# Optimization experiments

Measured on AMD Instinct MI355X. Metric: run time of the kernel, lower is better.

Reference implementation:

```python
import jax, jax.numpy as jnp
import numpy as np

T, B, E, F = 2048, 8, 512, 2
N = E * F  # state dim = emb_dim * exp_factor


def setup_inputs() -> dict:
    key = jax.random.key(0)
    ks = jax.random.split(key, 14)
    x = jax.random.normal(ks[0], (T, B, E), dtype=jnp.float32)
    # in/out projections (torch Linear: y = x @ W.T + b; we store W already transposed)
    W_in = jax.random.normal(ks[1], (E, N), dtype=jnp.float32) / np.sqrt(E)
    b_in = jnp.zeros((N,), dtype=jnp.float32)
    W_out = jax.random.normal(ks[2], (N, E), dtype=jnp.float32) / np.sqrt(N)
    b_out = jnp.zeros((E,), dtype=jnp.float32)
    # LRU eigenvalue parameterization (r_min=0, r_max=1)
    u1 = jax.random.uniform(ks[3], (N,), dtype=jnp.float32, minval=1e-4, maxval=1.0)
    u2 = jax.random.uniform(ks[4], (N,), dtype=jnp.float32)
    nu_log = jnp.log(-0.5 * jnp.log(u1))
    theta_log = jnp.log(u2 * 2.0 * np.pi)
    gamma_log = jnp.log(jnp.sqrt(1.0 - jnp.exp(-jnp.exp(nu_log)) ** 2))
    B_real = jax.random.normal(ks[5], (N, N), dtype=jnp.float32) / np.sqrt(2 * E)
    B_imag = jax.random.normal(ks[6], (N, N), dtype=jnp.float32) / np.sqrt(2 * N)
    C_real = jax.random.normal(ks[7], (N, N), dtype=jnp.float32) / np.sqrt(N)
    C_imag = jax.random.normal(ks[8], (N, N), dtype=jnp.float32) / np.sqrt(N)
    D = jax.random.normal(ks[9], (N,), dtype=jnp.float32)
    return {"x": x, "W_in": W_in, "b_in": b_in, "W_out": W_out, "b_out": b_out,
            "nu_log": nu_log, "theta_log": theta_log, "gamma_log": gamma_log,
            "B_real": B_real, "B_imag": B_imag, "C_real": C_real, "C_imag": C_imag,
            "D": D}


def _bin_op(el1, el2):
    a_i, bu_i = el1
    a_j, bu_j = el2
    return (a_j * a_i, a_j * bu_i + bu_j)


def reference(x, W_in, b_in, W_out, b_out, nu_log, theta_log, gamma_log,
              B_real, B_imag, C_real, C_imag, D):
    u = x @ W_in + b_in                                   # [T,B,N] real
    Lam = jnp.exp(-jnp.exp(nu_log) + 1j * jnp.exp(theta_log))        # [N] complex
    B_norm = (B_real + 1j * B_imag) * jnp.exp(gamma_log)[:, None]    # [N,N]
    C = C_real + 1j * C_imag                                          # [N,N]
    # Bu[t,b,j] = sum_i B_norm[i,j] * u[t,b,i]  (matches einsum 'ij,kmi->kmj')
    Bu = jnp.einsum('ij,tbi->tbj', B_norm, u.astype(B_norm.dtype))   # [T,B,N]
    Lam_elems = jnp.broadcast_to(Lam, Bu.shape)                       # [T,B,N]
    # linear recurrence h_t = Lam * h_{t-1} + Bu_t via associative scan over time (axis 0)
    _, h = jax.lax.associative_scan(_bin_op, (Lam_elems, Bu), axis=0)
    y = (jnp.einsum('ij,tbi->tbj', C, h) + D * u).real                # [T,B,N]
    return y @ W_out + b_out                                          # [T,B,E]
```

## Files before the change

### kernel.cpp

```cpp
#include <hip/hip_runtime.h>
#include <hip/hip_bf16.h>

typedef __hip_bfloat16 bf16;
typedef __attribute__((ext_vector_type(8))) short bf16x8;
typedef __attribute__((ext_vector_type(4))) float f32x4;

#define T_DIM 2048
#define B_DIM 8
#define E_DIM 512
#define N_DIM 1024
#define M_ROWS (T_DIM * B_DIM)
#define NCHUNK 64
#define CLEN (T_DIM / NCHUNK)

__device__ __forceinline__ void gload16(const void* g, void* l) {
    __builtin_amdgcn_global_load_lds((const void __attribute__((address_space(1)))*)g,
                                     (void __attribute__((address_space(3)))*)l, 16, 0, 0);
}

__global__ void k_prep(const float* __restrict__ nu_log, const float* __restrict__ theta_log,
                       const float* __restrict__ gamma_log,
                       float* __restrict__ LamR, float* __restrict__ LamI, float* __restrict__ g) {
    int i = blockIdx.x * 256 + threadIdx.x;
    if (i < N_DIM) {
        float nu  = expf(nu_log[i]);
        float th  = expf(theta_log[i]);
        float mag = expf(-nu);
        LamR[i] = mag * cosf(th);
        LamI[i] = mag * sinf(th);
        g[i] = expf(gamma_log[i]);
    }
}

struct __align__(8) bf4 { bf16 v[4]; };
__global__ void k_conv_all(const float* __restrict__ x, const float* __restrict__ W_in,
                           const float* __restrict__ C_r, const float* __restrict__ C_i,
                           bf16* __restrict__ xb, bf16* __restrict__ Win_b,
                           bf16* __restrict__ Cr_b, bf16* __restrict__ Ci_b) {
    int id = blockIdx.x;
    const float* src; bf16* dst; float mul = 1.f; int base;
    if (id < 8192)      { src = x;    dst = xb;    base = id; }
    else if (id < 8704) { src = W_in; dst = Win_b; base = id - 8192; }
    else if (id < 9728) { src = C_r;  dst = Cr_b;  base = id - 8704; }
    else                { src = C_i;  dst = Ci_b;  base = id - 9728; mul = -1.f; }
    int i = base * 256 + threadIdx.x;
    float4 v = ((const float4*)src)[i];
    bf4 o;
    o.v[0] = __float2bfloat16(v.x * mul);
    o.v[1] = __float2bfloat16(v.y * mul);
    o.v[2] = __float2bfloat16(v.z * mul);
    o.v[3] = __float2bfloat16(v.w * mul);
    ((bf4*)dst)[i] = o;
}

__global__ void k_transpose_all(const float* __restrict__ B_r, const float* __restrict__ B_i,
                                const float* __restrict__ W_out, const float* __restrict__ gvec,
                                const float* __restrict__ Dvec,
                                bf16* __restrict__ BscT, bf16* __restrict__ WoT,
                                bf16* __restrict__ WoTD) {
    __shared__ float tile[32][33];
    int id = blockIdx.x;
    const float* in; bf16* out; const float* scale; int R, C, bx, by;
    if (id < 1024)      { in = B_r;   out = BscT;                      scale = gvec; R = 1024; C = 1024; bx = id & 31;          by = id >> 5; }
    else if (id < 2048) { int l = id - 1024; in = B_i; out = BscT + (size_t)1024 * 1024; scale = gvec; R = 1024; C = 1024; bx = l & 31; by = l >> 5; }
    else if (id < 2560) { int l = id - 2048; in = W_out; out = WoT;    scale = nullptr; R = 1024; C = 512; bx = l & 15; by = l >> 4; }
    else                { int l = id - 2560; in = W_out; out = WoTD;   scale = Dvec;   R = 1024; C = 512; bx = l & 15; by = l >> 4; }
    int tx = threadIdx.x & 31, ty = threadIdx.x >> 5;
    int r0 = by * 32, c0 = bx * 32;
#pragma unroll
    for (int i = 0; i < 32; i += 8) {
        int r = r0 + ty + i;
        float v = in[(size_t)r * C + c0 + tx];
        if (scale) v *= scale[r];
        tile[ty + i][tx] = v;
    }
    __syncthreads();
#pragma unroll
    for (int i = 0; i < 32; i += 8) {
        out[(size_t)(c0 + ty + i) * R + r0 + tx] = __float2bfloat16(tile[tx][ty + i]);
    }
}

__global__ void k_bias_bu(const float* __restrict__ b_in, const float* __restrict__ g,
                          const float* __restrict__ B_real, const float* __restrict__ B_imag,
                          float* __restrict__ c_bu) {
    int id = blockIdx.x;
    int jblk = id & 7, ic = id >> 3;
    int j = jblk * 256 + threadIdx.x;
    const float* B = (j < N_DIM) ? B_real : B_imag;
    int jj = j & (N_DIM - 1);
    float s = 0.f;
    for (int i = ic * 128; i < ic * 128 + 128; ++i)
        s = fmaf(b_in[i] * g[i], B[(size_t)i * N_DIM + jj], s);
    atomicAdd(&c_bu[j], s);
}

__global__ void k_bias_out(const float* __restrict__ b_out, const float* __restrict__ b_in,
                           const float* __restrict__ D, const float* __restrict__ W_out,
                           float* __restrict__ bo) {
    int id = blockIdx.x;
    int eblk = id & 1, ic = id >> 1;
    int e = eblk * 256 + threadIdx.x;
    float s = (ic == 0) ? b_out[e] : 0.f;
    for (int j = ic * 128; j < ic * 128 + 128; ++j)
        s = fmaf(b_in[j] * D[j], W_out[(size_t)j * E_DIM + e], s);
    atomicAdd(&bo[e], s);
}

template <bool ASPLIT, bool OUTF32, bool BIAS>
__device__ __forceinline__ void gemm_db_core(bf16* lds,
        const bf16* __restrict__ A0, const bf16* __restrict__ A1, int ksplit,
        int lda0, int lda1, const bf16* __restrict__ Bt, int ldb,
        void* __restrict__ outp, int ldo, const float* __restrict__ bias, int K,
        int bn, int bm) {
    const int tid = threadIdx.x;
    const int lane = tid & 63, w = tid >> 6;
    const int wr = w >> 1, wc = w & 1;
    const int fr = lane & 15, fq = lane >> 4;
    f32x4 acc[4][4] = {};
    const int nt = K / 32;

    auto stage = [&](int buf, int t) {
        int k0 = t * 32;
        const bf16* Ap = A0; int lda = lda0, ac = k0;
        if (ASPLIT && k0 >= ksplit) { Ap = A1; lda = lda1; ac = k0 - ksplit; }
        bf16* dst = lds + buf * 8192;
#pragma unroll
        for (int L = 0; L < 2; ++L) {
            int idx = L * 256 + tid;
            int rr = idx >> 2, s = idx & 3;
            int kk = (s ^ (rr & 3)) * 8;
            gload16(Ap + (size_t)(bm * 128 + rr) * lda + ac + kk, dst + idx * 8);
            gload16(Bt + (size_t)(bn * 128 + rr) * ldb + k0 + kk, dst + 4096 + idx * 8);
        }
    };

    stage(0, 0);
    __syncthreads();
    int cur = 0;
    for (int t = 0; t < nt; ++t) {
        if (t + 1 < nt) stage(cur ^ 1, t + 1);
        const bf16* bufA = lds + cur * 8192;
        const bf16* bufB = bufA + 4096;
        bf16x8 af[4], bfr[4];
#pragma unroll
        for (int i = 0; i < 4; ++i) {
            int rr = wr * 64 + i * 16 + fr;
            af[i] = *(const bf16x8*)(bufA + (rr * 4 + (fq ^ (rr & 3))) * 8);
        }
#pragma unroll
        for (int j = 0; j < 4; ++j) {
            int rr = wc * 64 + j * 16 + fr;
            bfr[j] = *(const bf16x8*)(bufB + (rr * 4 + (fq ^ (rr & 3))) * 8);
        }
        __builtin_amdgcn_s_setprio(1);
#pragma unroll
        for (int i = 0; i < 4; ++i)
#pragma unroll
            for (int j = 0; j < 4; ++j)
                acc[i][j] = __builtin_amdgcn_mfma_f32_16x16x32_bf16(af[i], bfr[j], acc[i][j], 0, 0, 0);
        __builtin_amdgcn_s_setprio(0);
        __syncthreads();
        cur ^= 1;
    }
    const int orow = bm * 128 + wr * 64;
    const int ocol = bn * 128 + wc * 64;
#pragma unroll
    for (int i = 0; i < 4; ++i)
#pragma unroll
        for (int j = 0; j < 4; ++j) {
            int col = ocol + j * 16 + fr;
            float bv = BIAS ? bias[col] : 0.0f;
#pragma unroll
            for (int r = 0; r < 4; ++r) {
                int row = orow + i * 16 + fq * 4 + r;
                float v = acc[i][j][r] + bv;
                if (OUTF32) ((float*)outp)[(size_t)row * ldo + col] = v;
                else        ((bf16*)outp)[(size_t)row * ldo + col] = __float2bfloat16(v);
            }
        }
}

__global__ __launch_bounds__(256)
void k_g1(const bf16* __restrict__ xb, const bf16* __restrict__ WBcat,
          bf16* __restrict__ BuH, const float* __restrict__ c_bu) {
    __shared__ __align__(16) bf16 lds[2 * 8192];
    int id = blockIdx.x;
    int swz = (id & 7) * 256 + (id >> 3);
    int bn = swz & 15, bm = swz >> 4;
    gemm_db_core<false, false, true>(lds, xb, nullptr, 0, 512, 0, WBcat, 512,
                                     BuH, 2048, c_bu, 512, bn, bm);
}

__global__ __launch_bounds__(256)
void k_g2(const bf16* __restrict__ BuH, const bf16* __restrict__ xb,
          const bf16* __restrict__ Bfin, float* __restrict__ out,
          const float* __restrict__ biasO) {
    __shared__ __align__(16) bf16 lds[2 * 8192];
    int id = blockIdx.x;
    int swz = (id & 7) * 64 + (id >> 3);
    int bn = swz & 3, bm = swz >> 2;
    gemm_db_core<true, true, true>(lds, BuH, xb, 2048, 2048, 512, Bfin, 2560,
                                   out, 512, biasO, 2560, bn, bm);
}

__global__ __launch_bounds__(256)
void k_gemm4(const bf16* __restrict__ BscT, const bf16* __restrict__ Win_b,
             const bf16* __restrict__ WoT, const bf16* __restrict__ WoTD,
             const bf16* __restrict__ Cr_b, const bf16* __restrict__ Ci_b,
             bf16* __restrict__ WBcat, bf16* __restrict__ Bfin) {
    __shared__ __align__(16) bf16 lds[2 * 8192];
    int id = blockIdx.x;
    if (id < 64) {
        gemm_db_core<false, false, false>(lds, BscT, nullptr, 0, 1024, 0, Win_b, 1024, WBcat, 512, nullptr, 1024, id & 3, id >> 2);
    } else if (id < 96) {
        int l = id - 64;
        gemm_db_core<false, false, false>(lds, WoT, nullptr, 0, 1024, 0, Cr_b, 1024, Bfin, 2560, nullptr, 1024, l & 7, l >> 3);
    } else if (id < 128) {
        int l = id - 96;
        gemm_db_core<false, false, false>(lds, WoT, nullptr, 0, 1024, 0, Ci_b, 1024, Bfin + 1024, 2560, nullptr, 1024, l & 7, l >> 3);
    } else {
        int l = id - 128;
        gemm_db_core<false, false, false>(lds, WoTD, nullptr, 0, 1024, 0, Win_b, 1024, Bfin + 2048, 2560, nullptr, 1024, l & 3, l >> 2);
    }
}

__global__ void k_scan_carry(const bf16* __restrict__ BuH, const float* __restrict__ LamR,
                             const float* __restrict__ LamI, float2* __restrict__ carry) {
    int tid = blockIdx.x * 256 + threadIdx.x;
    int n = tid & (N_DIM - 1);
    int bb = (tid >> 10) & 7;
    int c = tid >> 13;
    float lr = LamR[n], li = LamI[n];
    float hr = 0.f, hi = 0.f;
    const bf16* p = BuH + ((size_t)(c * CLEN) * B_DIM + bb) * 2048 + n;
#pragma unroll 8
    for (int t = 0; t < CLEN; ++t) {
        float br = __bfloat162float(p[0]);
        float bi = __bfloat162float(p[N_DIM]);
        float nr = fmaf(lr, hr, fmaf(-li, hi, br));
        float ni = fmaf(lr, hi, fmaf(li, hr, bi));
        hr = nr; hi = ni;
        p += B_DIM * 2048;
    }
    carry[tid] = make_float2(hr, hi);
}

__global__ void k_scan_combine(const float2* __restrict__ carry, float2* __restrict__ S,
                               const float* __restrict__ LamR, const float* __restrict__ LamI) {
    int tid = blockIdx.x * 256 + threadIdx.x;
    int n = tid & (N_DIM - 1);
    float ar = LamR[n], ai = LamI[n];
#pragma unroll
    for (int s = 0; s < 5; ++s) { float nr = ar * ar - ai * ai, ni = 2.f * ar * ai; ar = nr; ai = ni; }
    float sr = 0.f, si = 0.f;
    for (int c = 0; c < NCHUNK; ++c) {
        S[(size_t)c * 8192 + tid] = make_float2(sr, si);
        float2 ca = carry[(size_t)c * 8192 + tid];
        float nr = fmaf(ar, sr, fmaf(-ai, si, ca.x));
        float ni = fmaf(ar, si, fmaf(ai, sr, ca.y));
        sr = nr; si = ni;
    }
}

__global__ void k_scan_apply(bf16* __restrict__ BuH, const float* __restrict__ LamR,
                             const float* __restrict__ LamI, const float2* __restrict__ S) {
    int tid = blockIdx.x * 256 + threadIdx.x;
    int n = tid & (N_DIM - 1);
    int bb = (tid >> 10) & 7;
    int c = tid >> 13;
    float lr = LamR[n], li = LamI[n];
    float2 s0 = S[tid];
    float hr = s0.x, hi = s0.y;
    bf16* p = BuH + ((size_t)(c * CLEN) * B_DIM + bb) * 2048 + n;
#pragma unroll 8
    for (int t = 0; t < CLEN; ++t) {
        float br = __bfloat162float(p[0]);
        float bi = __bfloat162float(p[N_DIM]);
        float nr = fmaf(lr, hr, fmaf(-li, hi, br));
        float ni = fmaf(lr, hi, fmaf(li, hr, bi));
        hr = nr; hi = ni;
        p[0] = __float2bfloat16(hr);
        p[N_DIM] = __float2bfloat16(hi);
        p += B_DIM * 2048;
    }
}

extern "C" void kernel_launch(void* const* d_in, const int* in_sizes, int n_in,
                              void* d_out, int out_size, void* d_ws, size_t ws_size,
                              hipStream_t stream) {
    const float* x         = (const float*)d_in[0];
    const float* W_in      = (const float*)d_in[1];
    const float* b_in      = (const float*)d_in[2];
    const float* W_out     = (const float*)d_in[3];
    const float* b_out     = (const float*)d_in[4];
    const float* nu_log    = (const float*)d_in[5];
    const float* theta_log = (const float*)d_in[6];
    const float* gamma_log = (const float*)d_in[7];
    const float* B_real    = (const float*)d_in[8];
    const float* B_imag    = (const float*)d_in[9];
    const float* C_real    = (const float*)d_in[10];
    const float* C_imag    = (const float*)d_in[11];
    const float* Dvec      = (const float*)d_in[12];
    float* out = (float*)d_out;

    char* ws = (char*)d_ws;
    size_t off = 0;
    auto alloc = [&](size_t bytes) { void* p = ws + off; off = (off + bytes + 255) & ~(size_t)255; return p; };
    bf16*  xb    = (bf16*)alloc((size_t)M_ROWS * E_DIM * 2);
    bf16*  BuH   = (bf16*)alloc((size_t)M_ROWS * 2048 * 2);
    bf16*  BscT  = (bf16*)alloc((size_t)2048 * 1024 * 2);
    bf16*  Win_b = (bf16*)alloc((size_t)512 * 1024 * 2);
    bf16*  Cr_b  = (bf16*)alloc((size_t)1024 * 1024 * 2);
    bf16*  Ci_b  = (bf16*)alloc((size_t)1024 * 1024 * 2);
    bf16*  WoT   = (bf16*)alloc((size_t)512 * 1024 * 2);
    bf16*  WoTD  = (bf16*)alloc((size_t)512 * 1024 * 2);
    bf16*  WBcat = (bf16*)alloc((size_t)2048 * 512 * 2);
    bf16*  Bfin  = (bf16*)alloc((size_t)512 * 2560 * 2);
    float* LamR  = (float*)alloc(1024 * 4);
    float* LamI  = (float*)alloc(1024 * 4);
    float* gvec  = (float*)alloc(1024 * 4);
    float* c_bu  = (float*)alloc(2048 * 4);
    float* biasO = (float*)alloc(512 * 4);
    float2* carry = (float2*)alloc((size_t)NCHUNK * 8192 * 8);
    float2* Sbuf  = (float2*)alloc((size_t)NCHUNK * 8192 * 8);

    k_prep<<<4, 256, 0, stream>>>(nu_log, theta_log, gamma_log, LamR, LamI, gvec);
    k_conv_all<<<10752, 256, 0, stream>>>(x, W_in, C_real, C_imag, xb, Win_b, Cr_b, Ci_b);
    k_transpose_all<<<3072, 256, 0, stream>>>(B_real, B_imag, W_out, gvec, Dvec, BscT, WoT, WoTD);

    hipMemsetAsync(c_bu, 0, 2048 * 4, stream);
    hipMemsetAsync(biasO, 0, 512 * 4, stream);
    k_bias_bu<<<64, 256, 0, stream>>>(b_in, gvec, B_real, B_imag, c_bu);
    k_bias_out<<<16, 256, 0, stream>>>(b_out, b_in, Dvec, W_out, biasO);

    k_gemm4<<<144, 256, 0, stream>>>(BscT, Win_b, WoT, WoTD, Cr_b, Ci_b, WBcat, Bfin);

    k_g1<<<2048, 256, 0, stream>>>(xb, WBcat, BuH, c_bu);

    k_scan_carry<<<NCHUNK * 8192 / 256, 256, 0, stream>>>(BuH, LamR, LamI, carry);
    k_scan_combine<<<32, 256, 0, stream>>>(carry, Sbuf, LamR, LamI);
    k_scan_apply<<<NCHUNK * 8192 / 256, 256, 0, stream>>>(BuH, LamR, LamI, Sbuf);

    k_g2<<<512, 256, 0, stream>>>(BuH, xb, Bfin, out, biasO);
}
```

Measured before the change: 339.2 us.

## Split-K the final GEMM with atomics, fuse bias kernels, change LDS swizzle

The final output GEMM (K=2560) is split into two K halves across 1024 blocks, with results accumulated into a zeroed fp32 output via atomicAdd. This is meant to raise occupancy, since the previous 512 blocks only partly filled the GPU. The prep kernel and both bias-vector kernels are merged into one launch, which recomputes exp(gamma) inline, and the LDS swizzle changes from XOR to an additive rotation. The cost is an extra memset of the output, fp32 atomic traffic, and a non-deterministic summation order.

```diff
diff --git a/kernel.cpp b/kernel.cpp
--- a/kernel.cpp
+++ b/kernel.cpp
@@ -18,17 +18,40 @@
                                      (void __attribute__((address_space(3)))*)l, 16, 0, 0);
 }
 
-__global__ void k_prep(const float* __restrict__ nu_log, const float* __restrict__ theta_log,
-                       const float* __restrict__ gamma_log,
-                       float* __restrict__ LamR, float* __restrict__ LamI, float* __restrict__ g) {
-    int i = blockIdx.x * 256 + threadIdx.x;
-    if (i < N_DIM) {
+__global__ void k_prep_bias(const float* __restrict__ nu_log, const float* __restrict__ theta_log,
+                            const float* __restrict__ gamma_log, const float* __restrict__ b_in,
+                            const float* __restrict__ B_real, const float* __restrict__ B_imag,
+                            const float* __restrict__ b_out, const float* __restrict__ Dvec,
+                            const float* __restrict__ W_out,
+                            float* __restrict__ LamR, float* __restrict__ LamI,
+                            float* __restrict__ g, float* __restrict__ c_bu, float* __restrict__ bo) {
+    int id = blockIdx.x;
+    if (id < 4) {
+        int i = id * 256 + threadIdx.x;
         float nu  = expf(nu_log[i]);
         float th  = expf(theta_log[i]);
         float mag = expf(-nu);
         LamR[i] = mag * cosf(th);
         LamI[i] = mag * sinf(th);
         g[i] = expf(gamma_log[i]);
+    } else if (id < 68) {
+        int l = id - 4;
+        int jblk = l & 7, ic = l >> 3;
+        int j = jblk * 256 + threadIdx.x;
+        const float* B = (j < N_DIM) ? B_real : B_imag;
+        int jj = j & (N_DIM - 1);
+        float s = 0.f;
+        for (int i = ic * 128; i < ic * 128 + 128; ++i)
+            s = fmaf(b_in[i] * expf(gamma_log[i]), B[(size_t)i * N_DIM + jj], s);
+        atomicAdd(&c_bu[j], s);
+    } else {
+        int l = id - 68;
+        int eblk = l & 1, ic = l >> 1;
+        int e = eblk * 256 + threadIdx.x;
+        float s = (ic == 0) ? b_out[e] : 0.f;
+        for (int j = ic * 128; j < ic * 128 + 128; ++j)
+            s = fmaf(b_in[j] * Dvec[j], W_out[(size_t)j * E_DIM + e], s);
+        atomicAdd(&bo[e], s);
     }
 }
 
@@ -81,47 +104,20 @@
     }
 }
 
-__global__ void k_bias_bu(const float* __restrict__ b_in, const float* __restrict__ g,
-                          const float* __restrict__ B_real, const float* __restrict__ B_imag,
-                          float* __restrict__ c_bu) {
-    int id = blockIdx.x;
-    int jblk = id & 7, ic = id >> 3;
-    int j = jblk * 256 + threadIdx.x;
-    const float* B = (j < N_DIM) ? B_real : B_imag;
-    int jj = j & (N_DIM - 1);
-    float s = 0.f;
-    for (int i = ic * 128; i < ic * 128 + 128; ++i)
-        s = fmaf(b_in[i] * g[i], B[(size_t)i * N_DIM + jj], s);
-    atomicAdd(&c_bu[j], s);
-}
-
-__global__ void k_bias_out(const float* __restrict__ b_out, const float* __restrict__ b_in,
-                           const float* __restrict__ D, const float* __restrict__ W_out,
-                           float* __restrict__ bo) {
-    int id = blockIdx.x;
-    int eblk = id & 1, ic = id >> 1;
-    int e = eblk * 256 + threadIdx.x;
-    float s = (ic == 0) ? b_out[e] : 0.f;
-    for (int j = ic * 128; j < ic * 128 + 128; ++j)
-        s = fmaf(b_in[j] * D[j], W_out[(size_t)j * E_DIM + e], s);
-    atomicAdd(&bo[e], s);
-}
-
-template <bool ASPLIT, bool OUTF32, bool BIAS>
+template <bool ASPLIT, bool OUTF32, bool BIAS, bool ATOMIC>
 __device__ __forceinline__ void gemm_db_core(bf16* lds,
         const bf16* __restrict__ A0, const bf16* __restrict__ A1, int ksplit,
         int lda0, int lda1, const bf16* __restrict__ Bt, int ldb,
-        void* __restrict__ outp, int ldo, const float* __restrict__ bias, int K,
-        int bn, int bm) {
+        void* __restrict__ outp, int ldo, const float* __restrict__ bias,
+        int kbase, int nt, int bn, int bm) {
     const int tid = threadIdx.x;
     const int lane = tid & 63, w = tid >> 6;
     const int wr = w >> 1, wc = w & 1;
     const int fr = lane & 15, fq = lane >> 4;
     f32x4 acc[4][4] = {};
-    const int nt = K / 32;
 
     auto stage = [&](int buf, int t) {
-        int k0 = t * 32;
+        int k0 = kbase + t * 32;
         const bf16* Ap = A0; int lda = lda0, ac = k0;
         if (ASPLIT && k0 >= ksplit) { Ap = A1; lda = lda1; ac = k0 - ksplit; }
         bf16* dst = lds + buf * 8192;
@@ -129,7 +125,7 @@
         for (int L = 0; L < 2; ++L) {
             int idx = L * 256 + tid;
             int rr = idx >> 2, s = idx & 3;
-            int kk = (s ^ (rr & 3)) * 8;
+            int kk = ((s - rr - (rr >> 2)) & 3) * 8;
             gload16(Ap + (size_t)(bm * 128 + rr) * lda + ac + kk, dst + idx * 8);
             gload16(Bt + (size_t)(bn * 128 + rr) * ldb + k0 + kk, dst + 4096 + idx * 8);
         }
@@ -146,12 +142,12 @@
 #pragma unroll
         for (int i = 0; i < 4; ++i) {
             int rr = wr * 64 + i * 16 + fr;
-            af[i] = *(const bf16x8*)(bufA + (rr * 4 + (fq ^ (rr & 3))) * 8);
+            af[i] = *(const bf16x8*)(bufA + (rr * 4 + ((fq + rr + (rr >> 2)) & 3)) * 8);
         }
 #pragma unroll
         for (int j = 0; j < 4; ++j) {
             int rr = wc * 64 + j * 16 + fr;
-            bfr[j] = *(const bf16x8*)(bufB + (rr * 4 + (fq ^ (rr & 3))) * 8);
+            bfr[j] = *(const bf16x8*)(bufB + (rr * 4 + ((fq + rr + (rr >> 2)) & 3)) * 8);
         }
         __builtin_amdgcn_s_setprio(1);
 #pragma unroll
@@ -170,13 +166,14 @@
 #pragma unroll
         for (int j = 0; j < 4; ++j) {
             int col = ocol + j * 16 + fr;
-            float bv = BIAS ? bias[col] : 0.0f;
+            float bv = (BIAS && bias) ? bias[col] : 0.0f;
 #pragma unroll
             for (int r = 0; r < 4; ++r) {
                 int row = orow + i * 16 + fq * 4 + r;
                 float v = acc[i][j][r] + bv;
-                if (OUTF32) ((float*)outp)[(size_t)row * ldo + col] = v;
-                else        ((bf16*)outp)[(size_t)row * ldo + col] = __float2bfloat16(v);
+                if (ATOMIC)      atomicAdd((float*)outp + (size_t)row * ldo + col, v);
+                else if (OUTF32) ((float*)outp)[(size_t)row * ldo + col] = v;
+                else             ((bf16*)outp)[(size_t)row * ldo + col] = __float2bfloat16(v);
             }
         }
 }
@@ -188,8 +185,8 @@
     int id = blockIdx.x;
     int swz = (id & 7) * 256 + (id >> 3);
     int bn = swz & 15, bm = swz >> 4;
-    gemm_db_core<false, false, true>(lds, xb, nullptr, 0, 512, 0, WBcat, 512,
-                                     BuH, 2048, c_bu, 512, bn, bm);
+    gemm_db_core<false, false, true, false>(lds, xb, nullptr, 0, 512, 0, WBcat, 512,
+                                            BuH, 2048, c_bu, 0, 16, bn, bm);
 }
 
 __global__ __launch_bounds__(256)
@@ -198,10 +195,13 @@
           const float* __restrict__ biasO) {
     __shared__ __align__(16) bf16 lds[2 * 8192];
     int id = blockIdx.x;
-    int swz = (id & 7) * 64 + (id >> 3);
+    int half = id >> 9;
+    int hid = id & 511;
+    int swz = (hid & 7) * 64 + (hid >> 3);
     int bn = swz & 3, bm = swz >> 2;
-    gemm_db_core<true, true, true>(lds, BuH, xb, 2048, 2048, 512, Bfin, 2560,
-                                   out, 512, biasO, 2560, bn, bm);
+    gemm_db_core<true, true, true, true>(lds, BuH, xb, 2048, 2048, 512, Bfin, 2560,
+                                         out, 512, half ? nullptr : biasO,
+                                         half * 1280, 40, bn, bm);
 }
 
 __global__ __launch_bounds__(256)
@@ -212,16 +212,16 @@
     __shared__ __align__(16) bf16 lds[2 * 8192];
     int id = blockIdx.x;
     if (id < 64) {
-        gemm_db_core<false, false, false>(lds, BscT, nullptr, 0, 1024, 0, Win_b, 1024, WBcat, 512, nullptr, 1024, id & 3, id >> 2);
+        gemm_db_core<false, false, false, false>(lds, BscT, nullptr, 0, 1024, 0, Win_b, 1024, WBcat, 512, nullptr, 0, 32, id & 3, id >> 2);
     } else if (id < 96) {
         int l = id - 64;
-        gemm_db_core<false, false, false>(lds, WoT, nullptr, 0, 1024, 0, Cr_b, 1024, Bfin, 2560, nullptr, 1024, l & 7, l >> 3);
+        gemm_db_core<false, false, false, false>(lds, WoT, nullptr, 0, 1024, 0, Cr_b, 1024, Bfin, 2560, nullptr, 0, 32, l & 7, l >> 3);
     } else if (id < 128) {
         int l = id - 96;
-        gemm_db_core<false, false, false>(lds, WoT, nullptr, 0, 1024, 0, Ci_b, 1024, Bfin + 1024, 2560, nullptr, 1024, l & 7, l >> 3);
+        gemm_db_core<false, false, false, false>(lds, WoT, nullptr, 0, 1024, 0, Ci_b, 1024, Bfin + 1024, 2560, nullptr, 0, 32, l & 7, l >> 3);
     } else {
         int l = id - 128;
-        gemm_db_core<false, false, false>(lds, WoTD, nullptr, 0, 1024, 0, Win_b, 1024, Bfin + 2048, 2560, nullptr, 1024, l & 3, l >> 2);
+        gemm_db_core<false, false, false, false>(lds, WoTD, nullptr, 0, 1024, 0, Win_b, 1024, Bfin + 2048, 2560, nullptr, 0, 32, l & 3, l >> 2);
     }
 }
 
@@ -325,14 +325,14 @@
     float2* carry = (float2*)alloc((size_t)NCHUNK * 8192 * 8);
     float2* Sbuf  = (float2*)alloc((size_t)NCHUNK * 8192 * 8);
 
-    k_prep<<<4, 256, 0, stream>>>(nu_log, theta_log, gamma_log, LamR, LamI, gvec);
+    hipMemsetAsync(c_bu, 0, 2048 * 4, stream);
+    hipMemsetAsync(biasO, 0, 512 * 4, stream);
+    hipMemsetAsync(out, 0, (size_t)M_ROWS * E_DIM * 4, stream);
+
+    k_prep_bias<<<84, 256, 0, stream>>>(nu_log, theta_log, gamma_log, b_in, B_real, B_imag,
+                                        b_out, Dvec, W_out, LamR, LamI, gvec, c_bu, biasO);
     k_conv_all<<<10752, 256, 0, stream>>>(x, W_in, C_real, C_imag, xb, Win_b, Cr_b, Ci_b);
     k_transpose_all<<<3072, 256, 0, stream>>>(B_real, B_imag, W_out, gvec, Dvec, BscT, WoT, WoTD);
-
-    hipMemsetAsync(c_bu, 0, 2048 * 4, stream);
-    hipMemsetAsync(biasO, 0, 512 * 4, stream);
-    k_bias_bu<<<64, 256, 0, stream>>>(b_in, gvec, B_real, B_imag, c_bu);
-    k_bias_out<<<16, 256, 0, stream>>>(b_out, b_in, Dvec, W_out, biasO);
 
     k_gemm4<<<144, 256, 0, stream>>>(BscT, Win_b, WoT, WoTD, Cr_b, Ci_b, WBcat, Bfin);
 
@@ -342,5 +342,5 @@
     k_scan_combine<<<32, 256, 0, stream>>>(carry, Sbuf, LamR, LamI);
     k_scan_apply<<<NCHUNK * 8192 / 256, 256, 0, stream>>>(BuH, LamR, LamI, Sbuf);
 
-    k_g2<<<512, 256, 0, stream>>>(BuH, xb, Bfin, out, biasO);
-}
+    k_g2<<<1024, 256, 0, stream>>>(BuH, xb, Bfin, out, biasO);
+}
```

New measurement: 380.5 us. 1.12x slower.
